# Kernel optimization log

Hardware: AMD Instinct MI355X
Metric: run time of the kernel (lower is better)

## Reference

```python
import jax, jax.numpy as jnp
import numpy as np

S = 8      # max segment id present in masks
D = 768    # hidden size (hardcoded in the torch module)
N_VIS = 100  # leading vision tokens in vision_trace_feat


def _segment_mean(feat, mask, n_seg):
    """Per-(batch, seg_id) mean of feat tokens where mask == seg_id.
    feat: [B, L, D], mask: [B, L] ints in 0..n_seg. Returns means [B, n_seg, D], counts [B, n_seg].
    Equivalent to the torch loop over seg_id + split + per-chunk mean(dim=0)."""
    onehot = (mask[:, :, None] == jnp.arange(1, n_seg + 1)[None, None, :]).astype(feat.dtype)  # [B,L,S]
    sums = jnp.einsum('bls,bld->bsd', onehot, feat)   # [B,S,D]
    counts = onehot.sum(axis=1)                        # [B,S]
    means = sums / jnp.maximum(counts, 1.0)[:, :, None]
    return means, counts


def setup_inputs() -> dict:
    key = jax.random.key(0)
    k1, k2, k3, k4, k5, k6 = jax.random.split(key, 6)
    B = 64
    vision_trace_feat = jax.random.normal(k1, (B, N_VIS + 412, D), dtype=jnp.float32)
    vision_trace_mask = jnp.sort(jax.random.randint(k2, (B, 412), 0, S + 1), axis=-1).astype(jnp.int32)
    caption_feat = jax.random.normal(k3, (B, 512, D), dtype=jnp.float32)
    caption_mask = jnp.sort(jax.random.randint(k4, (B, 513), 0, S + 1), axis=-1).astype(jnp.int32)
    vt_merge_w = jax.random.normal(k5, (2 * D, D), dtype=jnp.float32) * 0.02
    vt_merge_b = jax.random.normal(k6, (D,), dtype=jnp.float32) * 0.02
    return {
        'vision_trace_feat': vision_trace_feat,
        'vision_trace_mask': vision_trace_mask,
        'caption_feat': caption_feat,
        'caption_mask': caption_mask,
        'vt_merge_w': vt_merge_w,
        'vt_merge_b': vt_merge_b,
    }


def reference(vision_trace_feat, vision_trace_mask, caption_feat, caption_mask, vt_merge_w, vt_merge_b):
    # --- CaptionAggregator (meanpool) ---
    cm = caption_mask[:, 1:]                                   # drop CLS position
    c_means, c_counts = _segment_mean(caption_feat, cm, S)      # [B,S,D], [B,S]
    c_present = (c_counts > 0).astype(c_means.dtype)
    caption_out = c_means * c_present[:, :, None]               # dense form: empty segments zeroed

    # --- VisionTraceAggregator (meanpool) ---
    vision_feat = vision_trace_feat[:, :N_VIS].mean(axis=1)     # [B,D]
    trace_feat = vision_trace_feat[:, N_VIS:]                   # [B,Lt,D]
    t_means, t_counts = _segment_mean(trace_feat, vision_trace_mask, S)
    t_present = (t_counts > 0).astype(t_means.dtype)
    vt = jnp.concatenate(
        [t_means, jnp.broadcast_to(vision_feat[:, None, :], t_means.shape)], axis=-1)  # [B,S,2D]
    vt_out = (vt @ vt_merge_w + vt_merge_b) * t_present[:, :, None]
    return (caption_out, vt_out)
```

## Files before the change

### kernel.cpp

```cpp
#include <hip/hip_runtime.h>
#include <hip/hip_bf16.h>

#define SEGS   8
#define DIM    768
#define NVIS   100
#define BATCH  64
#define LTOK   512
#define NCHK   8
#define TPC    64

#define OFF_PCAP  0
#define OFF_PTRC  (OFF_PCAP + BATCH*NCHK*SEGS*DIM)
#define OFF_PVIS  (OFF_PTRC + BATCH*NCHK*SEGS*DIM)
#define OFF_PCCNT (OFF_PVIS + BATCH*2*DIM)
#define OFF_PTCNT (OFF_PCCNT + BATCH*NCHK*SEGS)
#define OFF_TMEAN (OFF_PTCNT + BATCH*NCHK*SEGS)
#define OFF_TCNT  (OFF_TMEAN + BATCH*9*DIM)


__global__ __launch_bounds__(192) void reduce_kernel(
    const float* __restrict__ vt_feat,
    const int* __restrict__ vt_mask,
    const float* __restrict__ cap_feat,
    const int* __restrict__ cap_mask,
    float* __restrict__ ws)
{
    const int bid  = blockIdx.x;
    const int type = bid >> 10;
    const int b    = (bid >> 4) & 63;
    const int ck   = (bid >> 1) & 7;
    const int half = bid & 1;
    const int tid  = threadIdx.x;
    const int c0   = half * 384 + tid * 2;

    __shared__ __align__(16) int msk[TPC];
    __shared__ int scnt[SEGS + 1];
    if (tid < SEGS + 1) scnt[tid] = 0;
    if (tid < TPC) {
        const int l = ck * TPC + tid;
        int m;
        if (type == 0) m = cap_mask[b * 513 + 1 + l];
        else           m = (l >= NVIS) ? vt_mask[b * 412 + (l - NVIS)] : 0;
        msk[tid] = m;
    }
    __syncthreads();
    if (half == 0 && tid < TPC) {
        const int m = msk[tid]; if (m > 0) atomicAdd(&scnt[m], 1);
    }

    float acc[SEGS][2];
#pragma unroll
    for (int s = 0; s < SEGS; ++s) { acc[s][0] = 0.f; acc[s][1] = 0.f; }
    float vacc[2] = {0.f, 0.f};
    float tmp[2]  = {0.f, 0.f};
    int cur = 0;

    const float* __restrict__ feat = (type == 0) ? cap_feat : vt_feat;
    const size_t base = (size_t)b * LTOK * DIM + (size_t)c0;

    for (int j = 0; j < TPC; j += 8) {
        const float* p = feat + base + (size_t)(ck * TPC + j) * DIM;
        float2 v[8];
#pragma unroll
        for (int u = 0; u < 8; ++u)
            v[u] = *reinterpret_cast<const float2*>(p + (size_t)u * DIM);
        const int4 m4a = *reinterpret_cast<const int4*>(&msk[j]);
        const int4 m4b = *reinterpret_cast<const int4*>(&msk[j + 4]);
        const int mm[8] = {m4a.x, m4a.y, m4a.z, m4a.w,
                           m4b.x, m4b.y, m4b.z, m4b.w};
#pragma unroll
        for (int u = 0; u < 8; ++u) {
            const int l = ck * TPC + j + u;
            if (type == 1 && l < NVIS) {
                vacc[0] += v[u].x; vacc[1] += v[u].y;
            } else {
                const int m = __builtin_amdgcn_readfirstlane(mm[u]);
                if (m != cur) {
#pragma unroll
                    for (int s = 0; s < SEGS; ++s)
                        if (cur == s + 1) {
                            acc[s][0] += tmp[0]; acc[s][1] += tmp[1];
                        }
                    tmp[0] = 0.f; tmp[1] = 0.f;
                    cur = m;
                }
                tmp[0] += v[u].x; tmp[1] += v[u].y;
            }
        }
    }
#pragma unroll
    for (int s = 0; s < SEGS; ++s)
        if (cur == s + 1) {
            acc[s][0] += tmp[0]; acc[s][1] += tmp[1];
        }

    __syncthreads();

    float* __restrict__ pbase = ws + (type == 0 ? OFF_PCAP : OFF_PTRC)
                              + ((size_t)(b * NCHK + ck) * SEGS) * DIM + c0;
#pragma unroll
    for (int s = 0; s < SEGS; ++s) {
        *reinterpret_cast<float2*>(pbase + s * DIM) =
            make_float2(acc[s][0], acc[s][1]);
    }
    if (half == 0) {
        int* __restrict__ cbase = (int*)(ws + (type == 0 ? OFF_PCCNT : OFF_PTCNT))
                                + (b * NCHK + ck) * SEGS;
        if (tid < SEGS) cbase[tid] = scnt[tid + 1];
    }
    if (type == 1 && ck < 2) {
        *reinterpret_cast<float2*>(ws + OFF_PVIS + (size_t)(b * 2 + ck) * DIM + c0) =
            make_float2(vacc[0], vacc[1]);
    }
}

__global__ __launch_bounds__(256) void combine1_kernel(
    const float* __restrict__ ws_c, float* __restrict__ ws,
    float* __restrict__ out)
{
    const int i = blockIdx.x * 256 + threadIdx.x;
    const int N1 = BATCH * SEGS * DIM / 4;
    if (i < N1) {
        const int b  = i / 1536;
        const int r  = i % 1536;
        const int s  = r / 192;
        const int d4 = (r % 192) * 4;
        float4 sum = make_float4(0.f, 0.f, 0.f, 0.f); int c = 0;
#pragma unroll
        for (int ck = 0; ck < NCHK; ++ck) {
            const float4 v = *reinterpret_cast<const float4*>(
                ws_c + OFF_PCAP + ((size_t)((b * NCHK + ck) * SEGS + s)) * DIM + d4);
            sum.x += v.x; sum.y += v.y; sum.z += v.z; sum.w += v.w;
            c += ((const int*)(ws_c + OFF_PCCNT))[(b * NCHK + ck) * SEGS + s];
        }
        float4 o = make_float4(0.f, 0.f, 0.f, 0.f);
        if (c > 0) {
            const float fc = (float)c;
            o = make_float4(sum.x / fc, sum.y / fc, sum.z / fc, sum.w / fc);
        }
        reinterpret_cast<float4*>(out)[i] = o;
    } else if (i < 2 * N1) {
        const int j  = i - N1;
        const int b  = j / 1536;
        const int r  = j % 1536;
        const int s  = r / 192;
        const int d4 = (r % 192) * 4;
        float4 sum = make_float4(0.f, 0.f, 0.f, 0.f); int c = 0;
#pragma unroll
        for (int ck = 0; ck < NCHK; ++ck) {
            const float4 v = *reinterpret_cast<const float4*>(
                ws_c + OFF_PTRC + ((size_t)((b * NCHK + ck) * SEGS + s)) * DIM + d4);
            sum.x += v.x; sum.y += v.y; sum.z += v.z; sum.w += v.w;
            c += ((const int*)(ws_c + OFF_PTCNT))[(b * NCHK + ck) * SEGS + s];
        }
        float4 m = make_float4(0.f, 0.f, 0.f, 0.f);
        if (c > 0) {
            const float fc = (float)c;
            m = make_float4(sum.x / fc, sum.y / fc, sum.z / fc, sum.w / fc);
        }
        *reinterpret_cast<float4*>(ws + OFF_TMEAN + ((size_t)(b * 9 + s)) * DIM + d4) = m;
        if (d4 == 0) ((int*)(ws + OFF_TCNT))[b * SEGS + s] = c;
    } else {
        const int j  = i - 2 * N1;
        const int b  = j / 192;
        const int d4 = (j % 192) * 4;
        const float4 v0 = *reinterpret_cast<const float4*>(
            ws_c + OFF_PVIS + (size_t)(b * 2 + 0) * DIM + d4);
        const float4 v1 = *reinterpret_cast<const float4*>(
            ws_c + OFF_PVIS + (size_t)(b * 2 + 1) * DIM + d4);
        const float sc = 1.0f / (float)NVIS;
        *reinterpret_cast<float4*>(ws + OFF_TMEAN + ((size_t)(b * 9 + 8)) * DIM + d4) =
            make_float4((v0.x + v1.x) * sc, (v0.y + v1.y) * sc,
                        (v0.z + v1.z) * sc, (v0.w + v1.w) * sc);
    }
}

__global__ __launch_bounds__(192) void gemm2_kernel(
    const float* __restrict__ W,
    const float* __restrict__ bias,
    const float* __restrict__ ws_c,
    float* __restrict__ out)
{
    const int b   = blockIdx.x >> 3;
    const int nc  = blockIdx.x & 7;
    const int n0  = nc * 96;
    const int tid = threadIdx.x;
    const int col = tid >> 1;
    const int kh  = tid & 1;
    const int d   = n0 + col;

    __shared__ __align__(16) float tm[9 * DIM];
    __shared__ float red[192][9];

    for (int idx = tid; idx < 9 * DIM / 4; idx += 192) {
        reinterpret_cast<float4*>(tm)[idx] =
            reinterpret_cast<const float4*>(ws_c + OFF_TMEAN + (size_t)b * 9 * DIM)[idx];
    }
    __syncthreads();

    float acc[9];
#pragma unroll
    for (int r = 0; r < 9; ++r) acc[r] = 0.f;

    const int k0 = kh * 384;
    const float* __restrict__ Wt = W + (size_t)k0 * DIM + d;
    const float* __restrict__ Wb = W + (size_t)(DIM + k0) * DIM + d;

    for (int k = 0; k < 384; k += 4) {
        float wt[4], wb[4];
#pragma unroll
        for (int u = 0; u < 4; ++u) {
            wt[u] = Wt[(size_t)(k + u) * DIM];
            wb[u] = Wb[(size_t)(k + u) * DIM];
        }
        float a[9][4];
#pragma unroll
        for (int r = 0; r < 9; ++r) {
            const float4 t = *reinterpret_cast<const float4*>(&tm[r * DIM + k0 + k]);
            a[r][0] = t.x; a[r][1] = t.y; a[r][2] = t.z; a[r][3] = t.w;
        }
#pragma unroll
        for (int u = 0; u < 4; ++u) {
#pragma unroll
            for (int r = 0; r < SEGS; ++r) acc[r] += a[r][u] * wt[u];
            acc[8] += a[8][u] * wb[u];
        }
    }

#pragma unroll
    for (int r = 0; r < 9; ++r) red[tid][r] = acc[r];
    __syncthreads();
    if (kh == 0) {
        float accT[9];
#pragma unroll
        for (int r = 0; r < 9; ++r) accT[r] = acc[r] + red[tid + 1][r];
        const float bs = bias[d];
        float* __restrict__ o = out + (size_t)BATCH * SEGS * DIM
                              + ((size_t)b * SEGS) * DIM + d;
#pragma unroll
        for (int s = 0; s < SEGS; ++s) {
            const int c = ((const int*)(ws_c + OFF_TCNT))[b * SEGS + s];
            o[(size_t)s * DIM] = (c > 0) ? (accT[s] + accT[8] + bs) : 0.f;
        }
    }
}

extern "C" void kernel_launch(void* const* d_in, const int* in_sizes, int n_in,
                              void* d_out, int out_size, void* d_ws, size_t ws_size,
                              hipStream_t stream) {
    const float* vt_feat  = (const float*)d_in[0];
    const int*   vt_mask  = (const int*)d_in[1];
    const float* cap_feat = (const float*)d_in[2];
    const int*   cap_mask = (const int*)d_in[3];
    const float* W        = (const float*)d_in[4];
    const float* bias     = (const float*)d_in[5];
    float* out = (float*)d_out;
    float* ws = (float*)d_ws;

    reduce_kernel  <<<2048, 192, 0, stream>>>(vt_feat, vt_mask, cap_feat, cap_mask, ws);
    combine1_kernel<<<816, 256, 0, stream>>>(ws, ws, out);
    gemm2_kernel   <<<512, 192, 0, stream>>>(W, bias, ws, out);
}
```

Before: 281.2 us.

## Retile merge GEMM to 4-column float4 threads with 8-way K split

```diff
diff --git a/kernel.cpp b/kernel.cpp
--- a/kernel.cpp
+++ b/kernel.cpp
@@ -185,63 +185,87 @@
     const int nc  = blockIdx.x & 7;
     const int n0  = nc * 96;
     const int tid = threadIdx.x;
-    const int col = tid >> 1;
-    const int kh  = tid & 1;
-    const int d   = n0 + col;
-
-    __shared__ __align__(16) float tm[9 * DIM];
-    __shared__ float red[192][9];
+    const int cg  = tid % 24;
+    const int kq  = tid / 24;
+    const int d0  = n0 + cg * 4;
+
+    __shared__ __align__(16) float tm[9 * 8 * 100];
+    __shared__ __align__(16) float red[192 * 9 * 4];
 
     for (int idx = tid; idx < 9 * DIM / 4; idx += 192) {
-        reinterpret_cast<float4*>(tm)[idx] =
-            reinterpret_cast<const float4*>(ws_c + OFF_TMEAN + (size_t)b * 9 * DIM)[idx];
-    }
-    __syncthreads();
-
-    float acc[9];
-#pragma unroll
-    for (int r = 0; r < 9; ++r) acc[r] = 0.f;
-
-    const int k0 = kh * 384;
-    const float* __restrict__ Wt = W + (size_t)k0 * DIM + d;
-    const float* __restrict__ Wb = W + (size_t)(DIM + k0) * DIM + d;
-
-    for (int k = 0; k < 384; k += 4) {
-        float wt[4], wb[4];
+        const int r   = idx / 192;
+        const int rem = idx % 192;
+        const int kq_ = rem / 24;
+        const int kk4 = rem % 24;
+        const float4 v = reinterpret_cast<const float4*>(
+            ws_c + OFF_TMEAN + (size_t)b * 9 * DIM)[idx];
+        *reinterpret_cast<float4*>(&tm[(r * 8 + kq_) * 100 + kk4 * 4]) = v;
+    }
+    __syncthreads();
+
+    float acc[9][4];
+#pragma unroll
+    for (int r = 0; r < 9; ++r) { acc[r][0]=0.f; acc[r][1]=0.f; acc[r][2]=0.f; acc[r][3]=0.f; }
+
+    const float* __restrict__ Wt = W + (size_t)(kq * 96) * DIM + d0;
+    const float* __restrict__ Wb = W + (size_t)(DIM + kq * 96) * DIM + d0;
+
+    for (int kk = 0; kk < 96; kk += 4) {
+        float4 wt[4], wb[4];
 #pragma unroll
         for (int u = 0; u < 4; ++u) {
-            wt[u] = Wt[(size_t)(k + u) * DIM];
-            wb[u] = Wb[(size_t)(k + u) * DIM];
+            wt[u] = *reinterpret_cast<const float4*>(Wt + (size_t)(kk + u) * DIM);
+            wb[u] = *reinterpret_cast<const float4*>(Wb + (size_t)(kk + u) * DIM);
         }
         float a[9][4];
 #pragma unroll
         for (int r = 0; r < 9; ++r) {
-            const float4 t = *reinterpret_cast<const float4*>(&tm[r * DIM + k0 + k]);
+            const float4 t = *reinterpret_cast<const float4*>(&tm[(r * 8 + kq) * 100 + kk]);
             a[r][0] = t.x; a[r][1] = t.y; a[r][2] = t.z; a[r][3] = t.w;
         }
 #pragma unroll
         for (int u = 0; u < 4; ++u) {
-#pragma unroll
-            for (int r = 0; r < SEGS; ++r) acc[r] += a[r][u] * wt[u];
-            acc[8] += a[8][u] * wb[u];
-        }
-    }
-
-#pragma unroll
-    for (int r = 0; r < 9; ++r) red[tid][r] = acc[r];
-    __syncthreads();
-    if (kh == 0) {
-        float accT[9];
-#pragma unroll
-        for (int r = 0; r < 9; ++r) accT[r] = acc[r] + red[tid + 1][r];
-        const float bs = bias[d];
-        float* __restrict__ o = out + (size_t)BATCH * SEGS * DIM
-                              + ((size_t)b * SEGS) * DIM + d;
-#pragma unroll
-        for (int s = 0; s < SEGS; ++s) {
-            const int c = ((const int*)(ws_c + OFF_TCNT))[b * SEGS + s];
-            o[(size_t)s * DIM] = (c > 0) ? (accT[s] + accT[8] + bs) : 0.f;
-        }
+            const float t4[4] = {wt[u].x, wt[u].y, wt[u].z, wt[u].w};
+            const float b4[4] = {wb[u].x, wb[u].y, wb[u].z, wb[u].w};
+#pragma unroll
+            for (int r = 0; r < SEGS; ++r) {
+#pragma unroll
+                for (int j = 0; j < 4; ++j) acc[r][j] += a[r][u] * t4[j];
+            }
+#pragma unroll
+            for (int j = 0; j < 4; ++j) acc[8][j] += a[8][u] * b4[j];
+        }
+    }
+
+#pragma unroll
+    for (int r = 0; r < 9; ++r)
+        *reinterpret_cast<float4*>(&red[(tid * 9 + r) * 4]) =
+            make_float4(acc[r][0], acc[r][1], acc[r][2], acc[r][3]);
+    __syncthreads();
+
+    {
+        const int cg2 = tid >> 3;
+        const int s   = tid & 7;
+        float4 sumS = make_float4(0.f, 0.f, 0.f, 0.f);
+        float4 sumV = make_float4(0.f, 0.f, 0.f, 0.f);
+#pragma unroll
+        for (int q = 0; q < 8; ++q) {
+            const int base = (q * 24 + cg2) * 9;
+            const float4 vS = *reinterpret_cast<const float4*>(&red[(base + s) * 4]);
+            const float4 vV = *reinterpret_cast<const float4*>(&red[(base + 8) * 4]);
+            sumS.x += vS.x; sumS.y += vS.y; sumS.z += vS.z; sumS.w += vS.w;
+            sumV.x += vV.x; sumV.y += vV.y; sumV.z += vV.z; sumV.w += vV.w;
+        }
+        const int dd = n0 + cg2 * 4;
+        const int c  = ((const int*)(ws_c + OFF_TCNT))[b * SEGS + s];
+        float4 o = make_float4(0.f, 0.f, 0.f, 0.f);
+        if (c > 0) {
+            const float4 bb = *reinterpret_cast<const float4*>(bias + dd);
+            o = make_float4(sumS.x + sumV.x + bb.x, sumS.y + sumV.y + bb.y,
+                            sumS.z + sumV.z + bb.z, sumS.w + sumV.w + bb.w);
+        }
+        *reinterpret_cast<float4*>(out + (size_t)BATCH * SEGS * DIM
+                                   + ((size_t)(b * SEGS + s)) * DIM + dd) = o;
     }
 }
 
```

Result: faster. 259.5 us (-7.7%).
